# Kernel tuning notes

Hardware: AMD Instinct MI355X
Metric: run time of the kernel (lower is better)

## Reference

```python
import jax, jax.numpy as jnp
import numpy as np

N, E, IN_F, EDGE_F, HID, S = 200000, 600000, 28, 4, 128, 20000
NUM_LAYERS = 4
L = NUM_LAYERS - 1
BN_EPS = 1e-5


def setup_inputs() -> dict:
    key = jax.random.key(0)
    ks = jax.random.split(key, 20)
    p = lambda k, shape: (jax.random.normal(k, shape, dtype=jnp.float32) * 0.1)
    return {
        'x': jax.random.normal(ks[0], (N, IN_F), dtype=jnp.float32),
        'edge_index': jax.random.randint(ks[1], (2, E), 0, N),
        'edge_attr': jax.random.normal(ks[2], (E, EDGE_F), dtype=jnp.float32),
        'edge_weight': jax.random.uniform(ks[3], (E,), dtype=jnp.float32),
        'node_mask': (jax.random.uniform(ks[4], (N,)) > 0.5).astype(jnp.float32),
        'subgraphs2nodes': jax.random.randint(ks[5], (N,), 0, S),
        # layer-1 params (in_features -> hidden)
        'be1_W1': p(ks[6], (EDGE_F, IN_F)), 'be1_b1': jnp.zeros((IN_F,), jnp.float32),
        'be1_W2': p(ks[7], (IN_F, IN_F)), 'be1_b2': jnp.zeros((IN_F,), jnp.float32),
        'm1_W1': p(ks[8], (IN_F, HID)), 'm1_b1': jnp.zeros((HID,), jnp.float32),
        'm1_W2': p(ks[9], (HID, HID)), 'm1_b2': jnp.zeros((HID,), jnp.float32),
        'bn1_g': jnp.ones((HID,), jnp.float32), 'bn1_b': jnp.zeros((HID,), jnp.float32),
        'eps1': jnp.zeros((), jnp.float32),
        # layers 2..NUM_LAYERS, stacked (hidden -> hidden)
        'beW1': p(ks[10], (L, EDGE_F, HID)), 'beb1': jnp.zeros((L, HID), jnp.float32),
        'beW2': p(ks[11], (L, HID, HID)), 'beb2': jnp.zeros((L, HID), jnp.float32),
        'mW1': p(ks[12], (L, HID, HID)), 'mb1': jnp.zeros((L, HID), jnp.float32),
        'mW2': p(ks[13], (L, HID, HID)), 'mb2': jnp.zeros((L, HID), jnp.float32),
        'bng': jnp.ones((L, HID), jnp.float32), 'bnb': jnp.zeros((L, HID), jnp.float32),
        'eps': jnp.zeros((L,), jnp.float32),
    }


def _mlp2(h, W1, b1, W2, b2):
    # Linear -> ReLU -> Linear
    return jnp.dot(jax.nn.relu(jnp.dot(h, W1) + b1), W2) + b2


def _gine(x, src, dst, edge_attr, edge_weight, eps,
          beW1, beb1, beW2, beb2, W1, b1, W2, b2, g, beta):
    # bond encoder on edge features
    e = _mlp2(edge_attr, beW1, beb1, beW2, beb2)            # [E, d]
    # message: relu(x_j + e_ij) * w_ij, aggregated at dst via scatter-add
    m = jax.nn.relu(x[src] + e) * edge_weight[:, None]      # [E, d]
    aggr = jax.ops.segment_sum(m, dst, num_segments=N)      # [N, d]
    h = (1.0 + eps) * x + aggr
    # node MLP: Linear,ReLU,Linear,BN(train mode),ReLU
    h = _mlp2(h, W1, b1, W2, b2)
    mu = jnp.mean(h, axis=0)
    var = jnp.mean((h - mu) ** 2, axis=0)
    h = (h - mu) * jax.lax.rsqrt(var + BN_EPS) * g + beta
    return jax.nn.relu(h)


def reference(x, edge_index, edge_attr, edge_weight, node_mask, subgraphs2nodes,
              be1_W1, be1_b1, be1_W2, be1_b2, m1_W1, m1_b1, m1_W2, m1_b2,
              bn1_g, bn1_b, eps1,
              beW1, beb1, beW2, beb2, mW1, mb1, mW2, mb2, bng, bnb, eps):
    src, dst = edge_index[0], edge_index[1]
    h = _gine(x, src, dst, edge_attr, edge_weight, eps1,
              be1_W1, be1_b1, be1_W2, be1_b2,
              m1_W1, m1_b1, m1_W2, m1_b2, bn1_g, bn1_b)
    for i in range(L):
        h_new = _gine(h, src, dst, edge_attr, edge_weight, eps[i],
                      beW1[i], beb1[i], beW2[i], beb2[i],
                      mW1[i], mb1[i], mW2[i], mb2[i], bng[i], bnb[i])
        h = h + h_new  # residual
    # float node_mask branch + global_add_pool over subgraphs2nodes
    h = h * node_mask[:, None]
    return jax.ops.segment_sum(h, subgraphs2nodes, num_segments=S)  # [S, HID]
```

## Files before the change

### kernel.cpp

```cpp
#include <hip/hip_runtime.h>
#include <hip/hip_bf16.h>


#define BNEPS 1e-5f
#define LDA 136
#define SCAN_NB 240

typedef __attribute__((ext_vector_type(8))) short bf16x8;
typedef __attribute__((ext_vector_type(8))) unsigned short u16x8;
typedef __attribute__((ext_vector_type(4))) float f32x4;

__device__ inline short f2bf(float f) {
    __hip_bfloat16 h = __float2bfloat16(f);
    return *reinterpret_cast<short*>(&h);
}
__device__ inline unsigned short f2bfu(float f) {
    __hip_bfloat16 h = __float2bfloat16(f);
    return *reinterpret_cast<unsigned short*>(&h);
}
__device__ inline float bf2f(unsigned short u) {
    union { unsigned int i; float f; } v; v.i = ((unsigned int)u) << 16; return v.f;
}

__global__ __launch_bounds__(256) void k_prep(
    const float* __restrict__ m1W2, const float* __restrict__ beW2,
    const float* __restrict__ mW1, const float* __restrict__ mW2,
    short* __restrict__ out)
{
    __shared__ float tileS[64][65];
    int b = blockIdx.x, mat = b >> 2, t = b & 3;
    const float* Wsrc;
    if (mat == 0) Wsrc = m1W2;
    else {
        int l = (mat - 1) / 3, which = (mat - 1) % 3;
        Wsrc = (which == 0) ? beW2 + (size_t)l * 16384
             : (which == 1) ? mW1 + (size_t)l * 16384
             :                mW2 + (size_t)l * 16384;
    }
    short* dst = out + (size_t)mat * 16384;
    int tr = (t >> 1) * 64, tc = (t & 1) * 64;
    for (int i = threadIdx.x; i < 4096; i += 256) {
        int r = i >> 6, c = i & 63;
        tileS[r][c] = Wsrc[(size_t)(tr + r) * 128 + (tc + c)];
    }
    __syncthreads();
    for (int i = threadIdx.x; i < 4096; i += 256) {
        int n = i >> 6, k = i & 63;
        dst[(size_t)(tc + n) * 128 + (tr + k)] = f2bf(tileS[k][n]);
    }
}

__global__ __launch_bounds__(256) void k_prep1(
    const float* __restrict__ W1, short* __restrict__ out)
{
    for (int i = threadIdx.x; i < 128 * 32; i += 256) {
        int n = i >> 5, k = i & 31;
        out[i] = (k < 28) ? f2bf(W1[(size_t)k * 128 + n]) : (short)0;
    }
}

__global__ __launch_bounds__(256) void k_prep28(
    const float* __restrict__ W2, short* __restrict__ out)
{
    for (int i = threadIdx.x; i < 32 * 32; i += 256) {
        int n = i >> 5, k = i & 31;
        out[i] = (n < 28 && k < 28) ? f2bf(W2[(size_t)k * 28 + n]) : (short)0;
    }
}

__global__ __launch_bounds__(256) void k_prepx(
    const float* __restrict__ x, unsigned short* __restrict__ xbf, int N)
{
    int total = N * 32;
    for (int i = blockIdx.x * 256 + threadIdx.x; i < total; i += gridDim.x * 256) {
        int n = i >> 5, c = i & 31;
        xbf[i] = (c < 28) ? f2bfu(x[(size_t)n * 28 + c]) : (unsigned short)0;
    }
}

__global__ __launch_bounds__(256) void k_count(
    const int* __restrict__ ei, int* __restrict__ counts, int E)
{
    for (int e = blockIdx.x * 256 + threadIdx.x; e < E; e += gridDim.x * 256)
        atomicAdd(&counts[ei[E + e]], 1);
}

__global__ __launch_bounds__(256) void k_count2(
    const int* __restrict__ s2n, const float* __restrict__ mask,
    int* __restrict__ counts2, int N)
{
    for (int n = blockIdx.x * 256 + threadIdx.x; n < N; n += gridDim.x * 256)
        if (mask[n] != 0.f) atomicAdd(&counts2[s2n[n]], 1);
}

__global__ __launch_bounds__(256) void k_scanA(
    const int* __restrict__ counts, int* __restrict__ bsum, int N, int seg)
{
    __shared__ int red[256];
    int b = blockIdx.x;
    int lo = b * seg, hi = min(lo + seg, N);
    int s = 0;
    for (int i = lo + threadIdx.x; i < hi; i += 256) s += counts[i];
    red[threadIdx.x] = s;
    __syncthreads();
    for (int d = 128; d > 0; d >>= 1) {
        if (threadIdx.x < d) red[threadIdx.x] += red[threadIdx.x + d];
        __syncthreads();
    }
    if (threadIdx.x == 0) bsum[b] = red[0];
// ... 18 lines not shown

__global__ __launch_bounds__(256) void k_scanC(
    const int* __restrict__ counts, const int* __restrict__ bsum,
    int* __restrict__ offs, int* __restrict__ cursor, int N, int seg)
{
    __shared__ int sh[256];
    int b = blockIdx.x;
    int lo = b * seg, hi = min(lo + seg, N);
    int base = bsum[b];
    for (int t0 = lo; t0 < hi; t0 += 256) {
        int i = t0 + threadIdx.x;
        int v = (i < hi) ? counts[i] : 0;
        sh[threadIdx.x] = v;
        __syncthreads();
        for (int d = 1; d < 256; d <<= 1) {
            int t = (threadIdx.x >= d) ? sh[threadIdx.x - d] : 0;
            __syncthreads();
            sh[threadIdx.x] += t;
            __syncthreads();
        }
        int excl = base + sh[threadIdx.x] - v;
        if (i < hi) { offs[i] = excl; cursor[i] = excl; }
        int tileTotal = sh[255];
        __syncthreads();
        base += tileTotal;
    }
}

__global__ __launch_bounds__(256) void k_scatter(
    const int* __restrict__ ei, const float* __restrict__ ew,
    const float4* __restrict__ ea4,
    int* __restrict__ cursor, int2* __restrict__ pmeta,
    float4* __restrict__ pea4, int E)
{
    for (int e = blockIdx.x * 256 + threadIdx.x; e < E; e += gridDim.x * 256) {
        int d = ei[E + e];
        int pos = atomicAdd(&cursor[d], 1);
        pmeta[pos] = make_int2(ei[e], __float_as_int(ew[e]));
        pea4[pos] = ea4[e];
    }
}

__global__ __launch_bounds__(256) void k_scatter2(
    const int* __restrict__ s2n, const float* __restrict__ mask,
    int* __restrict__ cursor2, int* __restrict__ perm2, int N)
{
    for (int n = blockIdx.x * 256 + threadIdx.x; n < N; n += gridDim.x * 256)
        if (mask[n] != 0.f) {
            int pos = atomicAdd(&cursor2[s2n[n]], 1);
            perm2[pos] = n;
        }
}

__global__ __launch_bounds__(256) void k_emsg(
    const float4* __restrict__ pea4,
    const float* __restrict__ W1, const float* __restrict__ b1,
    const short* __restrict__ W2t, const float* __restrict__ b2,
    unsigned short* __restrict__ emsg, const int* __restrict__ offs,
    int n0, int n1)
{
    __shared__ short Bs[128 * LDA];
    __shared__ short As[64 * LDA];
    __shared__ float eas[64][4];
    int e0 = offs[n0], e1 = offs[n1];
    int tid = threadIdx.x;
    for (int i = tid; i < 2048; i += 256) {
        int n = (i * 8) >> 7, k = (i * 8) & 127;
        *(bf16x8*)&Bs[n * LDA + k] = *(const bf16x8*)&W2t[i * 8];
    }
    int j = tid & 127, half = tid >> 7;
    float w10 = W1[j], w11 = W1[128 + j], w12 = W1[256 + j], w13 = W1[384 + j];
    float b1j = b1[j];
    int w = tid >> 6, lane = tid & 63;
    int l15 = lane & 15, quad = lane >> 4;
    __syncthreads();

    int numTiles = (e1 - e0 + 63) >> 6;
    for (int tile = blockIdx.x; tile < numTiles; tile += gridDim.x) {
        int base = e0 + tile * 64;
        __syncthreads();
        if (tid < 64) {
            int k = base + tid;
            float4 a = make_float4(0.f, 0.f, 0.f, 0.f);
            if (k < e1) a = pea4[k];
            eas[tid][0] = a.x; eas[tid][1] = a.y; eas[tid][2] = a.z; eas[tid][3] = a.w;
        }
        __syncthreads();
        #pragma unroll
        for (int q = 0; q < 32; ++q) {
            int e = half * 32 + q;
            float t = fmaf(eas[e][0], w10, fmaf(eas[e][1], w11,
                      fmaf(eas[e][2], w12, fmaf(eas[e][3], w13, b1j))));
            As[e * LDA + j] = f2bf(fmaxf(t, 0.f));
        }
        __syncthreads();
        f32x4 acc[8];
        #pragma unroll
        for (int nt = 0; nt < 8; ++nt) acc[nt] = (f32x4){0.f, 0.f, 0.f, 0.f};
        #pragma unroll
        for (int kt = 0; kt < 4; ++kt) {
            bf16x8 af = *(bf16x8*)&As[(w * 16 + l15) * LDA + kt * 32 + quad * 8];
            #pragma unroll
            for (int nt = 0; nt < 8; ++nt) {
                bf16x8 bf = *(bf16x8*)&Bs[(nt * 16 + l15) * LDA + kt * 32 + quad * 8];
                acc[nt] = __builtin_amdgcn_mfma_f32_16x16x32_bf16(af, bf, acc[nt], 0, 0, 0);
            }
        }
        #pragma unroll
        for (int nt = 0; nt < 8; ++nt) {
            int col = nt * 16 + l15;
            float b2c = b2[col];
            #pragma unroll
            for (int r = 0; r < 4; ++r) {
                int row = w * 16 + quad * 4 + r;
                As[row * LDA + col] = f2bf(acc[nt][r] + b2c);
            }
        }
        __syncthreads();
        #pragma unroll
        for (int kk = 0; kk < 4; ++kk) {
            int i = tid + kk * 256;
            int row = (i * 8) >> 7, col = (i * 8) & 127;
            int gr = base + row;
            if (gr < e1)
                *(bf16x8*)&emsg[(size_t)(gr - e0) * 128 + col] = *(bf16x8*)&As[row * LDA + col];
        }
    }
}

__global__ __launch_bounds__(256) void k_emsg28_mm(
    const float4* __restrict__ pea4,
    const float* __restrict__ W1, const float* __restrict__ b1,
    const short* __restrict__ W2t28,
    const float* __restrict__ b2,
    unsigned short* __restrict__ emsg28, int E)
{
    __shared__ short Bs[32 * 40];
    __shared__ short As[64 * 40];
    __shared__ float eas[64][4];
    __shared__ float b2s[32];
    int tid = threadIdx.x;
    for (int i = tid; i < 32 * 32; i += 256) {
        int n = i >> 5, k = i & 31;
        Bs[n * 40 + k] = W2t28[i];
    }
    if (tid < 32) b2s[tid] = (tid < 28) ? b2[tid] : 0.f;
    int j = tid & 31, sub = tid >> 5;
    float w10 = 0.f, w11 = 0.f, w12 = 0.f, w13 = 0.f, b1j = 0.f;
    if (j < 28) { w10 = W1[j]; w11 = W1[28 + j]; w12 = W1[56 + j]; w13 = W1[84 + j]; b1j = b1[j]; }
    int w = tid >> 6, lane = tid & 63;
    int l15 = lane & 15, quad = lane >> 4;
    __syncthreads();

    int numTiles = (E + 63) >> 6;
    for (int tile = blockIdx.x; tile < numTiles; tile += gridDim.x) {
        int base = tile * 64;
        __syncthreads();
        if (tid < 64) {
            int k = base + tid;
            float4 a = (k < E) ? pea4[k] : make_float4(0.f, 0.f, 0.f, 0.f);
            eas[tid][0] = a.x; eas[tid][1] = a.y; eas[tid][2] = a.z; eas[tid][3] = a.w;
        }
        __syncthreads();
        #pragma unroll
        for (int q = 0; q < 8; ++q) {
            int e = q * 8 + sub;
            float t = fmaf(eas[e][0], w10, fmaf(eas[e][1], w11,
                      fmaf(eas[e][2], w12, fmaf(eas[e][3], w13, b1j))));
            As[e * 40 + j] = (j < 28) ? f2bf(fmaxf(t, 0.f)) : (short)0;
        }
        __syncthreads();
        f32x4 acc[2];
        acc[0] = (f32x4){0.f, 0.f, 0.f, 0.f};
        acc[1] = (f32x4){0.f, 0.f, 0.f, 0.f};
        bf16x8 af = *(bf16x8*)&As[(w * 16 + l15) * 40 + quad * 8];
        #pragma unroll
        for (int nt = 0; nt < 2; ++nt) {
            bf16x8 bf = *(bf16x8*)&Bs[(nt * 16 + l15) * 40 + quad * 8];
// ... 20 lines not shown
__global__ __launch_bounds__(256) void k_gather(
    const unsigned short* __restrict__ h, const int* __restrict__ offs,
    const int2* __restrict__ pmeta, const unsigned short* __restrict__ emsg,
    unsigned short* __restrict__ a0,
    const float* __restrict__ epsp, int epsIdx,
    int n0, int n1)
{
    int grp = threadIdx.x >> 5, lane = threadIdx.x & 31;
    int n = n0 + blockIdx.x * 8 + grp;
    if (n >= n1) return;
    int e0 = offs[n0];
    int k0 = offs[n], k1 = offs[n + 1];
    float s = 1.0f + epsp[epsIdx];
    ushort4 hv0 = *(const ushort4*)&h[(size_t)n * 128 + lane * 4];
    float m0 = s * bf2f(hv0.x), m1 = s * bf2f(hv0.y);
    float m2 = s * bf2f(hv0.z), m3 = s * bf2f(hv0.w);
    for (int k = k0; k < k1; ++k) {
        int2 mt = pmeta[k];
        float w = __int_as_float(mt.y);
        ushort4 ev = *(const ushort4*)&emsg[(size_t)(k - e0) * 128 + lane * 4];
        ushort4 hv = *(const ushort4*)&h[(size_t)mt.x * 128 + lane * 4];
        m0 += fmaxf(bf2f(hv.x) + bf2f(ev.x), 0.f) * w;
        m1 += fmaxf(bf2f(hv.y) + bf2f(ev.y), 0.f) * w;
        m2 += fmaxf(bf2f(hv.z) + bf2f(ev.z), 0.f) * w;
        m3 += fmaxf(bf2f(hv.w) + bf2f(ev.w), 0.f) * w;
    }
    ushort4 o;
    o.x = f2bfu(m0); o.y = f2bfu(m1); o.z = f2bfu(m2); o.w = f2bfu(m3);
    *(ushort4*)&a0[(size_t)n * 128 + lane * 4] = o;
}

__global__ __launch_bounds__(256) void k_gather28(
    const float* __restrict__ x, const unsigned short* __restrict__ xbf,
    const int* __restrict__ offs,
    const int2* __restrict__ pmeta, const unsigned short* __restrict__ emsg28,
    const float* __restrict__ eps1, float* __restrict__ u28, int N)
{
    int grp = threadIdx.x >> 5, lane = threadIdx.x & 31;
    int n = blockIdx.x * 8 + grp;
    if (n >= N || lane >= 28) return;
    float s = 1.0f + eps1[0];
    int k0 = offs[n], k1 = offs[n + 1];
    float m = 0.f;
    for (int k = k0; k < k1; ++k) {
        int2 mt = pmeta[k];
        float w = __int_as_float(mt.y);
        float e = bf2f(emsg28[(size_t)k * 28 + lane]);
        float xs = bf2f(xbf[(size_t)mt.x * 32 + lane]);
        m += fmaxf(xs + e, 0.f) * w;
    }
    u28[(size_t)n * 28 + lane] = fmaf(s, x[(size_t)n * 28 + lane], m);
}

__global__ __launch_bounds__(512) void k_mlp(
    const unsigned short* __restrict__ src, const short* __restrict__ Wt1,
    const float* __restrict__ b1, const short* __restrict__ Wt2,
    const float* __restrict__ b2, unsigned short* __restrict__ dst,
    float* __restrict__ stats, int N)
{
    __shared__ short Bs1[128 * LDA];
    __shared__ short Bs2[128 * LDA];
    __shared__ short As[128 * LDA];
    __shared__ float sstat[256];
    int tid = threadIdx.x;
    for (int i = tid; i < 2048; i += 512) {
        int n = (i * 8) >> 7, k = (i * 8) & 127;
        *(bf16x8*)&Bs1[n * LDA + k] = *(const bf16x8*)&Wt1[i * 8];
        *(bf16x8*)&Bs2[n * LDA + k] = *(const bf16x8*)&Wt2[i * 8];
    }
    if (tid < 256) sstat[tid] = 0.f;
    int w = tid >> 6, lane = tid & 63;
    int l15 = lane & 15, quad = lane >> 4;
    int cg = w >> 2;
    int rb = (w & 3) * 32;
    __syncthreads();

    bf16x8 B1f[4][4], B2f[4][4];
    float b1r[4], b2r[4];
    #pragma unroll
    for (int nt = 0; nt < 4; ++nt) {
        int col = cg * 64 + nt * 16 + l15;
        b1r[nt] = b1[col]; b2r[nt] = b2[col];
        #pragma unroll
        for (int kt = 0; kt < 4; ++kt) {
            B1f[nt][kt] = *(bf16x8*)&Bs1[col * LDA + kt * 32 + quad * 8];
            B2f[nt][kt] = *(bf16x8*)&Bs2[col * LDA + kt * 32 + quad * 8];
        }
    }
    float lsum[2][4], lsq[2][4];
    #pragma unroll
    for (int rg = 0; rg < 2; ++rg)
        #pragma unroll
        for (int nt = 0; nt < 4; ++nt) { lsum[rg][nt] = 0.f; lsq[rg][nt] = 0.f; }

    int numTiles = (N + 127) >> 7;
    for (int tile = blockIdx.x; tile < numTiles; tile += gridDim.x) {
        int base = tile * 128;
        __syncthreads();
        #pragma unroll
        for (int kk = 0; kk < 4; ++kk) {
            int i = tid + kk * 512;
            int row = (i * 8) >> 7, col = (i * 8) & 127;
            int rr = base + row;
            bf16x8 v;
            if (rr < N) v = *(const bf16x8*)&src[(size_t)rr * 128 + col];
            else        v = (bf16x8){0,0,0,0,0,0,0,0};
            *(bf16x8*)&As[row * LDA + col] = v;
        }
        __syncthreads();
        f32x4 acc[2][4];
        #pragma unroll
        for (int rg = 0; rg < 2; ++rg)
            #pragma unroll
            for (int nt = 0; nt < 4; ++nt) acc[rg][nt] = (f32x4){0.f, 0.f, 0.f, 0.f};
        #pragma unroll
        for (int rg = 0; rg < 2; ++rg) {
            #pragma unroll
            for (int kt = 0; kt < 4; ++kt) {
                bf16x8 af = *(bf16x8*)&As[(rb + rg * 16 + l15) * LDA + kt * 32 + quad * 8];
                #pragma unroll
                for (int nt = 0; nt < 4; ++nt)
                    acc[rg][nt] = __builtin_amdgcn_mfma_f32_16x16x32_bf16(af, B1f[nt][kt], acc[rg][nt], 0, 0, 0);
            }
        }
        __syncthreads();
        #pragma unroll
        for (int rg = 0; rg < 2; ++rg)
            #pragma unroll
            for (int nt = 0; nt < 4; ++nt) {
                int col = cg * 64 + nt * 16 + l15;
                #pragma unroll
                for (int r = 0; r < 4; ++r)
                    As[(rb + rg * 16 + quad * 4 + r) * LDA + col] =
                        f2bf(fmaxf(acc[rg][nt][r] + b1r[nt], 0.f));
            }
        __syncthreads();
        #pragma unroll
        for (int rg = 0; rg < 2; ++rg)
            #pragma unroll
            for (int nt = 0; nt < 4; ++nt) acc[rg][nt] = (f32x4){0.f, 0.f, 0.f, 0.f};
        #pragma unroll
        for (int rg = 0; rg < 2; ++rg) {
            #pragma unroll
            for (int kt = 0; kt < 4; ++kt) {
                bf16x8 af = *(bf16x8*)&As[(rb + rg * 16 + l15) * LDA + kt * 32 + quad * 8];
                #pragma unroll
                for (int nt = 0; nt < 4; ++nt)
                    acc[rg][nt] = __builtin_amdgcn_mfma_f32_16x16x32_bf16(af, B2f[nt][kt], acc[rg][nt], 0, 0, 0);
            }
        }
        __syncthreads();
        #pragma unroll
        for (int rg = 0; rg < 2; ++rg)
            #pragma unroll
            for (int nt = 0; nt < 4; ++nt) {
                int col = cg * 64 + nt * 16 + l15;
                int row0 = base + rb + rg * 16 + quad * 4;
                #pragma unroll
                for (int r = 0; r < 4; ++r) {
                    float z = acc[rg][nt][r] + b2r[nt];
                    if (row0 + r < N) { lsum[rg][nt] += z; lsq[rg][nt] = fmaf(z, z, lsq[rg][nt]); }
                    As[(rb + rg * 16 + quad * 4 + r) * LDA + col] = f2bf(z);
                }
            }
        __syncthreads();
        #pragma unroll
        for (int kk = 0; kk < 4; ++kk) {
            int i = tid + kk * 512;
            int row = (i * 8) >> 7, col = (i * 8) & 127;
            int rr = base + row;
            if (rr < N)
                *(bf16x8*)&dst[(size_t)rr * 128 + col] = *(bf16x8*)&As[row * LDA + col];
        }
    }
    #pragma unroll
    for (int nt = 0; nt < 4; ++nt) {
        int col = cg * 64 + nt * 16 + l15;
        atomicAdd(&sstat[col], lsum[0][nt] + lsum[1][nt]);
        atomicAdd(&sstat[128 + col], lsq[0][nt] + lsq[1][nt]);
    }
    __syncthreads();
    if (tid < 256) atomicAdd(&stats[tid], sstat[tid]);
}

__global__ __launch_bounds__(512) void k_mlp1(
    const float* __restrict__ u28, const short* __restrict__ Wt1p,
    const float* __restrict__ b1, const short* __restrict__ Wt2,
    const float* __restrict__ b2, unsigned short* __restrict__ dst,
    float* __restrict__ stats, int N)
{
    __shared__ short Bs1[128 * 40];
    __shared__ short Bs2[128 * LDA];
    __shared__ short As[128 * LDA];
    __shared__ short A28[128 * 40];
    __shared__ float sstat[256];
    int tid = threadIdx.x;
    for (int i = tid; i < 128 * 32; i += 512) {
        int n = i >> 5, k = i & 31;
        Bs1[n * 40 + k] = Wt1p[i];
    }
    for (int i = tid; i < 2048; i += 512) {
        int n = (i * 8) >> 7, k = (i * 8) & 127;
        *(bf16x8*)&Bs2[n * LDA + k] = *(const bf16x8*)&Wt2[i * 8];
    }
    {
        int r = tid >> 2, c = tid & 3;
        if (r < 128) A28[r * 40 + 28 + c] = 0;
    }
    if (tid < 256) sstat[tid] = 0.f;
    int w = tid >> 6, lane = tid & 63;
    int l15 = lane & 15, quad = lane >> 4;
    int cg = w >> 2, rb = (w & 3) * 32;
    __syncthreads();

    bf16x8 B1f[4], B2f[4][4];
    float b1r[4], b2r[4];
    #pragma unroll
    for (int nt = 0; nt < 4; ++nt) {
        int col = cg * 64 + nt * 16 + l15;
        b1r[nt] = b1[col]; b2r[nt] = b2[col];
        B1f[nt] = *(bf16x8*)&Bs1[col * 40 + quad * 8];
        #pragma unroll
        for (int kt = 0; kt < 4; ++kt)
            B2f[nt][kt] = *(bf16x8*)&Bs2[col * LDA + kt * 32 + quad * 8];
    }
    float lsum[2][4], lsq[2][4];
    #pragma unroll
    for (int rg = 0; rg < 2; ++rg)
        #pragma unroll
        for (int nt = 0; nt < 4; ++nt) { lsum[rg][nt] = 0.f; lsq[rg][nt] = 0.f; }

    int numTiles = (N + 127) >> 7;
    for (int tile = blockIdx.x; tile < numTiles; tile += gridDim.x) {
        int base = tile * 128;
        __syncthreads();
        for (int i = tid; i < 128 * 28; i += 512) {
            int row = i / 28, col = i - row * 28;
            int rr = base + row;
            A28[row * 40 + col] = (rr < N) ? f2bf(u28[(size_t)rr * 28 + col]) : (short)0;
        }
        __syncthreads();
        f32x4 acc[2][4];
        #pragma unroll
        for (int rg = 0; rg < 2; ++rg)
            #pragma unroll
            for (int nt = 0; nt < 4; ++nt) acc[rg][nt] = (f32x4){0.f, 0.f, 0.f, 0.f};
        #pragma unroll
        for (int rg = 0; rg < 2; ++rg) {
            bf16x8 af = *(bf16x8*)&A28[(rb + rg * 16 + l15) * 40 + quad * 8];
            #pragma unroll
            for (int nt = 0; nt < 4; ++nt)
                acc[rg][nt] = __builtin_amdgcn_mfma_f32_16x16x32_bf16(af, B1f[nt], acc[rg][nt], 0, 0, 0);
        }
        #pragma unroll
        for (int rg = 0; rg < 2; ++rg)
            #pragma unroll
            for (int nt = 0; nt < 4; ++nt) {
                int col = cg * 64 + nt * 16 + l15;
                #pragma unroll
                for (int r = 0; r < 4; ++r)
                    As[(rb + rg * 16 + quad * 4 + r) * LDA + col] =
                        f2bf(fmaxf(acc[rg][nt][r] + b1r[nt], 0.f));
            }
        __syncthreads();
        #pragma unroll
        for (int rg = 0; rg < 2; ++rg)
            #pragma unroll
            for (int nt = 0; nt < 4; ++nt) acc[rg][nt] = (f32x4){0.f, 0.f, 0.f, 0.f};
        #pragma unroll
        for (int rg = 0; rg < 2; ++rg) {
            #pragma unroll
            for (int kt = 0; kt < 4; ++kt) {
                bf16x8 af = *(bf16x8*)&As[(rb + rg * 16 + l15) * LDA + kt * 32 + quad * 8];
                #pragma unroll
                for (int nt = 0; nt < 4; ++nt)
                    acc[rg][nt] = __builtin_amdgcn_mfma_f32_16x16x32_bf16(af, B2f[nt][kt], acc[rg][nt], 0, 0, 0);
            }
        }
        __syncthreads();
        #pragma unroll
        for (int rg = 0; rg < 2; ++rg)
            #pragma unroll
            for (int nt = 0; nt < 4; ++nt) {
                int col = cg * 64 + nt * 16 + l15;
                int row0 = base + rb + rg * 16 + quad * 4;
                #pragma unroll
                for (int r = 0; r < 4; ++r) {
                    float z = acc[rg][nt][r] + b2r[nt];
                    if (row0 + r < N) { lsum[rg][nt] += z; lsq[rg][nt] = fmaf(z, z, lsq[rg][nt]); }
                    As[(rb + rg * 16 + quad * 4 + r) * LDA + col] = f2bf(z);
                }
            }
        __syncthreads();
        #pragma unroll
        for (int kk = 0; kk < 4; ++kk) {
            int i = tid + kk * 512;
            int row = (i * 8) >> 7, col = (i * 8) & 127;
            int rr = base + row;
            if (rr < N)
                *(bf16x8*)&dst[(size_t)rr * 128 + col] = *(bf16x8*)&As[row * LDA + col];
        }
    }
    #pragma unroll
    for (int nt = 0; nt < 4; ++nt) {
        int col = cg * 64 + nt * 16 + l15;
        atomicAdd(&sstat[col], lsum[0][nt] + lsum[1][nt]);
        atomicAdd(&sstat[128 + col], lsq[0][nt] + lsq[1][nt]);
    }
    __syncthreads();
    if (tid < 256) atomicAdd(&stats[tid], sstat[tid]);
}

__global__ __launch_bounds__(128) void k_stats(
    const float* __restrict__ stats, const float* __restrict__ g,
    const float* __restrict__ b, float* __restrict__ ss, float invN)
{
    int j = threadIdx.x;
    float mu  = stats[j] * invN;
    float var = fmaf(stats[128 + j], invN, -mu * mu);
    float sc  = rsqrtf(fmaxf(var, 0.f) + BNEPS) * g[j];
    ss[j] = sc;
    ss[128 + j] = fmaf(-mu, sc, b[j]);
}

__global__ __launch_bounds__(256) void k_bn(
    const unsigned short* __restrict__ z, const float* __restrict__ ss,
    unsigned short* __restrict__ h, int residual, int N)
{
    int idx8 = blockIdx.x * 256 + threadIdx.x;
    int stride = gridDim.x * 256;
    int c0 = (idx8 & 15) * 8;
    float scl[8], sht[8];
    #pragma unroll
    for (int r = 0; r < 8; ++r) { scl[r] = ss[c0 + r]; sht[r] = ss[128 + c0 + r]; }
    int total8 = N * 16;
    for (; idx8 < total8; idx8 += stride) {
        int n = idx8 >> 4;
        u16x8 z8 = *(const u16x8*)&z[(size_t)n * 128 + c0];
        float hn[8];
        #pragma unroll
        for (int r = 0; r < 8; ++r)
            hn[r] = fmaxf(fmaf(bf2f(z8[r]), scl[r], sht[r]), 0.f);
        if (residual) {
            u16x8 h8 = *(const u16x8*)&h[(size_t)n * 128 + c0];
            #pragma unroll
            for (int r = 0; r < 8; ++r) hn[r] += bf2f(h8[r]);
        }
        u16x8 o;
        #pragma unroll
        for (int r = 0; r < 8; ++r) o[r] = f2bfu(hn[r]);
        *(u16x8*)&h[(size_t)n * 128 + c0] = o;
    }
}

__global__ __launch_bounds__(256) void k_poolbn(
    const unsigned short* __restrict__ z, const unsigned short* __restrict__ hprev,
    const float* __restrict__ ss, const int* __restrict__ offs2,
    const int* __restrict__ perm2, float* __restrict__ out, int S)
{
    int w = threadIdx.x >> 6, lane = threadIdx.x & 63;
// ... 77 lines not shown
    if (ws_size < need) return;

    unsigned short* h    = (unsigned short*)(ws + offH);
    unsigned short* a0   = (unsigned short*)(ws + offA0);
    unsigned short* emsg = (unsigned short*)(ws + offEm);
    float* u28    = (float*)(ws + offA0);
    unsigned short* xbf = (unsigned short*)(ws + offA0 + 26214400);
    float* stats  = (float*)(ws + offStats);
    float* ssbuf  = (float*)(ws + offSS);
    short* wts    = (short*)(ws + offWts);
    short* w1p    = wts + 10 * 16384;
    short* w2p28  = w1p + 4096;
    int*   counts = (int*)(ws + offCounts);
    int*   offs   = (int*)(ws + offOffs);
    int*   cursor = (int*)(ws + offCursor);
    int2*  pmeta  = (int2*)(ws + offPmeta);
    float4* pea4  = (float4*)(ws + offPea);
    int*   bsum   = (int*)(ws + offBsum);
    int*   cnt2   = (int*)(ws + offCnt2);
    int*   offs2  = (int*)(ws + offOffs2);
    int*   cur2   = (int*)(ws + offCur2);
    int*   perm2  = (int*)(ws + offPerm2);
    const float4* ea4 = (const float4*)ea;

    hipMemsetAsync(stats, 0, 4 * 256 * sizeof(float), stream);
    hipMemsetAsync(counts, 0, (size_t)N * sizeof(int), stream);
    hipMemsetAsync(cnt2, 0, (size_t)S * sizeof(int), stream);

    k_prep<<<40, 256, 0, stream>>>(m1W2, beW2, mW1, mW2, wts);
    k_prep1<<<1, 256, 0, stream>>>(m1W1, w1p);
    k_prep28<<<1, 256, 0, stream>>>(be1W2, w2p28);
    k_prepx<<<512, 256, 0, stream>>>(x, xbf, N);

    const int seg = (N + SCAN_NB - 1) / SCAN_NB;
    k_count<<<1024, 256, 0, stream>>>(ei, counts, E);
    k_scanA<<<SCAN_NB, 256, 0, stream>>>(counts, bsum, N, seg);
    k_scanB<<<1, 256, 0, stream>>>(bsum, SCAN_NB, offs, N);
    k_scanC<<<SCAN_NB, 256, 0, stream>>>(counts, bsum, offs, cursor, N, seg);
    k_scatter<<<1024, 256, 0, stream>>>(ei, ew, ea4, cursor, pmeta, pea4, E);

    const int seg2 = (S + SCAN_NB - 1) / SCAN_NB;
    k_count2<<<512, 256, 0, stream>>>(s2n, mask, cnt2, N);
    k_scanA<<<SCAN_NB, 256, 0, stream>>>(cnt2, bsum, S, seg2);
    k_scanB<<<1, 256, 0, stream>>>(bsum, SCAN_NB, offs2, S);
    k_scanC<<<SCAN_NB, 256, 0, stream>>>(cnt2, bsum, offs2, cur2, S, seg2);
    k_scatter2<<<512, 256, 0, stream>>>(s2n, mask, cur2, perm2, N);

    auto wt_be = [&](int l) { return wts + (size_t)(1 + 3 * l + 0) * 16384; };
    auto wt_m1 = [&](int l) { return wts + (size_t)(1 + 3 * l + 1) * 16384; };
    auto wt_m2 = [&](int l) { return wts + (size_t)(1 + 3 * l + 2) * 16384; };

    k_emsg28_mm<<<2048, 256, 0, stream>>>(pea4, be1W1, be1b1, w2p28, be1b2, emsg, E);
    k_gather28<<<(N + 7) / 8, 256, 0, stream>>>(x, xbf, offs, pmeta, emsg, eps1, u28, N);
    k_mlp1<<<512, 512, 0, stream>>>(u28, w1p, m1b1, wts , m1b2, h, stats, N);
    k_stats<<<1, 128, 0, stream>>>(stats, bn1g, bn1b, ssbuf, invN);
    k_bn<<<2048, 256, 0, stream>>>(h, ssbuf, h, 0, N);

    for (int l = 0; l < 3; ++l) {
        for (int c = 0; c < 2; ++c) {
            int n0 = (c == 0) ? 0 : NS;
            int n1 = (c == 0) ? NS : N;
            k_emsg<<<2048, 256, 0, stream>>>(pea4,
                beW1 + (size_t)l * 512, beb1 + (size_t)l * 128,
                wt_be(l), beb2 + (size_t)l * 128, emsg, offs, n0, n1);
            k_gather<<<(n1 - n0 + 7) / 8, 256, 0, stream>>>(h, offs, pmeta, emsg, a0,
                epsL, l, n0, n1);
        }
        k_mlp<<<512, 512, 0, stream>>>(a0, wt_m1(l), mb1 + (size_t)l * 128,
                                       wt_m2(l), mb2 + (size_t)l * 128, a0,
                                       stats + 256 * (l + 1), N);
        k_stats<<<1, 128, 0, stream>>>(stats + 256 * (l + 1),
            bng + (size_t)l * 128, bnb + (size_t)l * 128, ssbuf, invN);
        if (l < 2) {
            k_bn<<<2048, 256, 0, stream>>>(a0, ssbuf, h, 1, N);
        }
    }

    k_poolbn<<<(S + 3) / 4, 256, 0, stream>>>(a0, h, ssbuf, offs2, perm2,
                                              (float*)d_out, S);
}
```

Before: 1.041 ms.

## Pre-swizzle weights into MFMA fragment order and restructure MLP/edge-encoder kernels

Weights are rewritten at prep time into the exact per-lane MFMA B-fragment order, so kernels copy them linearly into LDS and read conflict-free contiguous fragments instead of keeping them in registers or using padded rows. The node MLP kernels now have each wave own 32 full rows across all 128 columns, double-buffer the next tile's input in registers, and drop most block barriers because waves only touch their own rows. The edge encoder computes the first layer per wave via shuffles with no shared staging or barriers. Grid sizes are halved for 256-row tiles and occupancy hints are added, at the cost of more registers and larger LDS footprint.

Result: no change. 1.030 ms (-1.1%).

```diff
diff --git a/kernel.cpp b/kernel.cpp
--- a/kernel.cpp
+++ b/kernel.cpp
@@ -21,6 +21,7 @@
 __device__ inline float bf2f(unsigned short u) {
     union { unsigned int i; float f; } v; v.i = ((unsigned int)u) << 16; return v.f;
 }
+
 
 __global__ __launch_bounds__(256) void k_prep(
     const float* __restrict__ m1W2, const float* __restrict__ beW2,
@@ -45,16 +46,20 @@
     }
     __syncthreads();
     for (int i = threadIdx.x; i < 4096; i += 256) {
-        int n = i >> 6, k = i & 63;
-        dst[(size_t)(tc + n) * 128 + (tr + k)] = f2bf(tileS[k][n]);
+        int kl = i & 63, nl = i >> 6;
+        int n = tc + nl, k = tr + kl;
+        int fo = (((n >> 4) * 4 + (k >> 5)) * 64 + (((k >> 3) & 3) * 16 + (n & 15))) * 8 + (k & 7);
+        dst[fo] = f2bf(tileS[kl][nl]);
     }
 }
 
 __global__ __launch_bounds__(256) void k_prep1(
     const float* __restrict__ W1, short* __restrict__ out)
 {
-    for (int i = threadIdx.x; i < 128 * 32; i += 256) {
-        int n = i >> 5, k = i & 31;
+    for (int i = threadIdx.x; i < 4096; i += 256) {
+        int j = i & 7, sub = (i >> 3) & 63, nt = i >> 9;
+        int quad = sub >> 4, l15 = sub & 15;
+        int n = nt * 16 + l15, k = quad * 8 + j;
         out[i] = (k < 28) ? f2bf(W1[(size_t)k * 128 + n]) : (short)0;
     }
 }
@@ -179,78 +184,73 @@
         }
 }
 
-__global__ __launch_bounds__(256) void k_emsg(
+__global__ __launch_bounds__(256, 3) void k_emsg(
     const float4* __restrict__ pea4,
     const float* __restrict__ W1, const float* __restrict__ b1,
-    const short* __restrict__ W2t, const float* __restrict__ b2,
+    const short* __restrict__ W2f, const float* __restrict__ b2,
     unsigned short* __restrict__ emsg, const int* __restrict__ offs,
     int n0, int n1)
 {
-    __shared__ short Bs[128 * LDA];
     __shared__ short As[64 * LDA];
-    __shared__ float eas[64][4];
+    __shared__ short Bs[16384];
     int e0 = offs[n0], e1 = offs[n1];
     int tid = threadIdx.x;
-    for (int i = tid; i < 2048; i += 256) {
-        int n = (i * 8) >> 7, k = (i * 8) & 127;
-        *(bf16x8*)&Bs[n * LDA + k] = *(const bf16x8*)&W2t[i * 8];
-    }
-    int j = tid & 127, half = tid >> 7;
-    float w10 = W1[j], w11 = W1[128 + j], w12 = W1[256 + j], w13 = W1[384 + j];
-    float b1j = b1[j];
     int w = tid >> 6, lane = tid & 63;
     int l15 = lane & 15, quad = lane >> 4;
+    int rb = w * 16;
+    for (int i = tid; i < 2048; i += 256)
+        *(bf16x8*)&Bs[i * 8] = *(const bf16x8*)&W2f[i * 8];
+    int c2 = lane * 2;
+    float w1a[4], w1b[4];
+    #pragma unroll
+    for (int a = 0; a < 4; ++a) { w1a[a] = W1[a * 128 + c2]; w1b[a] = W1[a * 128 + c2 + 1]; }
+    float b1a = b1[c2], b1b = b1[c2 + 1];
+    float b2r[8];
+    #pragma unroll
+    for (int nt = 0; nt < 8; ++nt) b2r[nt] = b2[nt * 16 + l15];
     __syncthreads();
 
+    const float* peaf = (const float*)pea4;
     int numTiles = (e1 - e0 + 63) >> 6;
     for (int tile = blockIdx.x; tile < numTiles; tile += gridDim.x) {
         int base = e0 + tile * 64;
-        __syncthreads();
-        if (tid < 64) {
-            int k = base + tid;
-            float4 a = make_float4(0.f, 0.f, 0.f, 0.f);
-            if (k < e1) a = pea4[k];
-            eas[tid][0] = a.x; eas[tid][1] = a.y; eas[tid][2] = a.z; eas[tid][3] = a.w;
-        }
-        __syncthreads();
-        #pragma unroll
-        for (int q = 0; q < 32; ++q) {
-            int e = half * 32 + q;
-            float t = fmaf(eas[e][0], w10, fmaf(eas[e][1], w11,
-                      fmaf(eas[e][2], w12, fmaf(eas[e][3], w13, b1j))));
-            As[e * LDA + j] = f2bf(fmaxf(t, 0.f));
-        }
-        __syncthreads();
+        int eidx = base + rb + (lane >> 2);
+        float v = (eidx < e1) ? peaf[(size_t)(base + rb) * 4 + lane] : 0.f;
+        #pragma unroll
+        for (int e = 0; e < 16; ++e) {
+            float a0v = __shfl(v, e * 4 + 0);
+            float a1v = __shfl(v, e * 4 + 1);
+            float a2v = __shfl(v, e * 4 + 2);
+            float a3v = __shfl(v, e * 4 + 3);
+            float t0 = fmaf(a0v, w1a[0], fmaf(a1v, w1a[1], fmaf(a2v, w1a[2], fmaf(a3v, w1a[3], b1a))));
+            float t1 = fmaf(a0v, w1b[0], fmaf(a1v, w1b[1], fmaf(a2v, w1b[2], fmaf(a3v, w1b[3], b1b))));
+            unsigned int pk = ((unsigned int)f2bfu(fmaxf(t1, 0.f)) << 16) | f2bfu(fmaxf(t0, 0.f));
+        *(unsigned int*)&As[(rb + e) * LDA + c2] = pk;
+        }
         f32x4 acc[8];
         #pragma unroll
         for (int nt = 0; nt < 8; ++nt) acc[nt] = (f32x4){0.f, 0.f, 0.f, 0.f};
         #pragma unroll
         for (int kt = 0; kt < 4; ++kt) {
-            bf16x8 af = *(bf16x8*)&As[(w * 16 + l15) * LDA + kt * 32 + quad * 8];
+            bf16x8 af = *(bf16x8*)&As[(rb + l15) * LDA + kt * 32 + quad * 8];
             #pragma unroll
             for (int nt = 0; nt < 8; ++nt) {
-                bf16x8 bf = *(bf16x8*)&Bs[(nt * 16 + l15) * LDA + kt * 32 + quad * 8];
+                bf16x8 bf = *(const bf16x8*)&Bs[((nt * 4 + kt) * 64 + lane) * 8];
                 acc[nt] = __builtin_amdgcn_mfma_f32_16x16x32_bf16(af, bf, acc[nt], 0, 0, 0);
             }
         }
         #pragma unroll
         for (int nt = 0; nt < 8; ++nt) {
-            int col = nt * 16 + l15;
-            float b2c = b2[col];
-            #pragma unroll
-            for (int r = 0; r < 4; ++r) {
-                int row = w * 16 + quad * 4 + r;
-                As[row * LDA + col] = f2bf(acc[nt][r] + b2c);
-            }
-        }
-        __syncthreads();
-        #pragma unroll
-        for (int kk = 0; kk < 4; ++kk) {
-            int i = tid + kk * 256;
-            int row = (i * 8) >> 7, col = (i * 8) & 127;
-            int gr = base + row;
+            #pragma unroll
+            for (int r = 0; r < 4; ++r)
+                As[(rb + quad * 4 + r) * LDA + nt * 16 + l15] = f2bf(acc[nt][r] + b2r[nt]);
+        }
+        #pragma unroll
+        for (int it = 0; it < 4; ++it) {
+            int arow = rb + it * 4 + quad;
+            int gr = base + arow;
             if (gr < e1)
-                *(bf16x8*)&emsg[(size_t)(gr - e0) * 128 + col] = *(bf16x8*)&As[row * LDA + col];
+                *(bf16x8*)&emsg[(size_t)(gr - e0) * 128 + l15 * 8] = *(bf16x8*)&As[arow * LDA + l15 * 8];
         }
     }
 }
@@ -377,260 +377,268 @@
     u28[(size_t)n * 28 + lane] = fmaf(s, x[(size_t)n * 28 + lane], m);
 }
 
-__global__ __launch_bounds__(512) void k_mlp(
-    const unsigned short* __restrict__ src, const short* __restrict__ Wt1,
-    const float* __restrict__ b1, const short* __restrict__ Wt2,
+__global__ __launch_bounds__(512, 2) void k_mlp(
+    const unsigned short* __restrict__ src, const short* __restrict__ W1f,
+    const float* __restrict__ b1, const short* __restrict__ W2f,
     const float* __restrict__ b2, unsigned short* __restrict__ dst,
     float* __restrict__ stats, int N)
 {
-    __shared__ short Bs1[128 * LDA];
-    __shared__ short Bs2[128 * LDA];
-    __shared__ short As[128 * LDA];
+    __shared__ short As[256 * LDA];
+    __shared__ short Bs1[16384];
+    __shared__ short Bs2[16384];
     __shared__ float sstat[256];
     int tid = threadIdx.x;
     for (int i = tid; i < 2048; i += 512) {
-        int n = (i * 8) >> 7, k = (i * 8) & 127;
-        *(bf16x8*)&Bs1[n * LDA + k] = *(const bf16x8*)&Wt1[i * 8];
-        *(bf16x8*)&Bs2[n * LDA + k] = *(const bf16x8*)&Wt2[i * 8];
+        *(bf16x8*)&Bs1[i * 8] = *(const bf16x8*)&W1f[i * 8];
+        *(bf16x8*)&Bs2[i * 8] = *(const bf16x8*)&W2f[i * 8];
     }
     if (tid < 256) sstat[tid] = 0.f;
     int w = tid >> 6, lane = tid & 63;
     int l15 = lane & 15, quad = lane >> 4;
-    int cg = w >> 2;
-    int rb = (w & 3) * 32;
+    int rb = w * 32;
+    float b1r[8], b2r[8], lsum[8], lsq[8];
+    #pragma unroll
+    for (int nt = 0; nt < 8; ++nt) {
+        b1r[nt] = b1[nt * 16 + l15]; b2r[nt] = b2[nt * 16 + l15];
+        lsum[nt] = 0.f; lsq[nt] = 0.f;
+    }
+    int numTiles = (N + 255) >> 8;
+    bf16x8 st[8];
+    {
+        int tile = blockIdx.x;
+        if (tile < numTiles) {
+            int base = tile * 256;
+            #pragma unroll
+            for (int kk = 0; kk < 8; ++kk) {
+                int i = tid + kk * 512;
+                int rr = base + (i >> 4);
+                st[kk] = (rr < N) ? *(const bf16x8*)&src[(size_t)rr * 128 + (i & 15) * 8]
+                                  : (bf16x8){0, 0, 0, 0, 0, 0, 0, 0};
+            }
+        }
+    }
     __syncthreads();
 
-    bf16x8 B1f[4][4], B2f[4][4];
-    float b1r[4], b2r[4];
-    #pragma unroll
-    for (int nt = 0; nt < 4; ++nt) {
-        int col = cg * 64 + nt * 16 + l15;
-        b1r[nt] = b1[col]; b2r[nt] = b2[col];
+    for (int tile = blockIdx.x; tile < numTiles; tile += gridDim.x) {
+        int base = tile * 256;
+        #pragma unroll
+        for (int kk = 0; kk < 8; ++kk) {
+            int i = tid + kk * 512;
+            *(bf16x8*)&As[(i >> 4) * LDA + (i & 15) * 8] = st[kk];
+        }
+        int tnext = tile + gridDim.x;
+        if (tnext < numTiles) {
+            int bn = tnext * 256;
+            #pragma unroll
+            for (int kk = 0; kk < 8; ++kk) {
+                int i = tid + kk * 512;
+                int rr = bn + (i >> 4);
+                st[kk] = (rr < N) ? *(const bf16x8*)&src[(size_t)rr * 128 + (i & 15) * 8]
+                                  : (bf16x8){0, 0, 0, 0, 0, 0, 0, 0};
+            }
+        }
+        __syncthreads();
+        f32x4 acc[2][8];
+        #pragma unroll
+        for (int rg = 0; rg < 2; ++rg)
+            #pragma unroll
+            for (int nt = 0; nt < 8; ++nt) acc[rg][nt] = (f32x4){0.f, 0.f, 0.f, 0.f};
         #pragma unroll
         for (int kt = 0; kt < 4; ++kt) {
-            B1f[nt][kt] = *(bf16x8*)&Bs1[col * LDA + kt * 32 + quad * 8];
-            B2f[nt][kt] = *(bf16x8*)&Bs2[col * LDA + kt * 32 + quad * 8];
-        }
-    }
-    float lsum[2][4], lsq[2][4];
-    #pragma unroll
-    for (int rg = 0; rg < 2; ++rg)
-        #pragma unroll
-        for (int nt = 0; nt < 4; ++nt) { lsum[rg][nt] = 0.f; lsq[rg][nt] = 0.f; }
-
-    int numTiles = (N + 127) >> 7;
-    for (int tile = blockIdx.x; tile < numTiles; tile += gridDim.x) {
-        int base = tile * 128;
-        __syncthreads();
-        #pragma unroll
-        for (int kk = 0; kk < 4; ++kk) {
-            int i = tid + kk * 512;
-            int row = (i * 8) >> 7, col = (i * 8) & 127;
-            int rr = base + row;
-            bf16x8 v;
-            if (rr < N) v = *(const bf16x8*)&src[(size_t)rr * 128 + col];
-            else        v = (bf16x8){0,0,0,0,0,0,0,0};
-            *(bf16x8*)&As[row * LDA + col] = v;
-        }
-        __syncthreads();
-        f32x4 acc[2][4];
+            bf16x8 af0 = *(bf16x8*)&As[(rb + l15) * LDA + kt * 32 + quad * 8];
+            bf16x8 af1 = *(bf16x8*)&As[(rb + 16 + l15) * LDA + kt * 32 + quad * 8];
+            #pragma unroll
+            for (int nt = 0; nt < 8; ++nt) {
+                bf16x8 bf = *(const bf16x8*)&Bs1[((nt * 4 + kt) * 64 + lane) * 8];
+                acc[0][nt] = __builtin_amdgcn_mfma_f32_16x16x32_bf16(af0, bf, acc[0][nt], 0, 0, 0);
+                acc[1][nt] = __builtin_amdgcn_mfma_f32_16x16x32_bf16(af1, bf, acc[1][nt], 0, 0, 0);
+            }
+        }
         #pragma unroll
         for (int rg = 0; rg < 2; ++rg)
             #pragma unroll
-            for (int nt = 0; nt < 4; ++nt) acc[rg][nt] = (f32x4){0.f, 0.f, 0.f, 0.f};
-        #pragma unroll
-        for (int rg = 0; rg < 2; ++rg) {
-            #pragma unroll
-            for (int kt = 0; kt < 4; ++kt) {
-                bf16x8 af = *(bf16x8*)&As[(rb + rg * 16 + l15) * LDA + kt * 32 + quad * 8];
-                #pragma unroll
-                for (int nt = 0; nt < 4; ++nt)
-                    acc[rg][nt] = __builtin_amdgcn_mfma_f32_16x16x32_bf16(af, B1f[nt][kt], acc[rg][nt], 0, 0, 0);
-            }
-        }
-        __syncthreads();
-        #pragma unroll
-        for (int rg = 0; rg < 2; ++rg)
-            #pragma unroll
-            for (int nt = 0; nt < 4; ++nt) {
-                int col = cg * 64 + nt * 16 + l15;
+            for (int nt = 0; nt < 8; ++nt)
                 #pragma unroll
                 for (int r = 0; r < 4; ++r)
-                    As[(rb + rg * 16 + quad * 4 + r) * LDA + col] =
+                    As[(rb + rg * 16 + quad * 4 + r) * LDA + nt * 16 + l15] =
                         f2bf(fmaxf(acc[rg][nt][r] + b1r[nt], 0.f));
-            }
-        __syncthreads();
         #pragma unroll
         for (int rg = 0; rg < 2; ++rg)
             #pragma unroll
-            for (int nt = 0; nt < 4; ++nt) acc[rg][nt] = (f32x4){0.f, 0.f, 0.f, 0.f};
-        #pragma unroll
-        for (int rg = 0; rg < 2; ++rg) {
-            #pragma unroll
-            for (int kt = 0; kt < 4; ++kt) {
-                bf16x8 af = *(bf16x8*)&As[(rb + rg * 16 + l15) * LDA + kt * 32 + quad * 8];
-                #pragma unroll
-                for (int nt = 0; nt < 4; ++nt)
-                    acc[rg][nt] = __builtin_amdgcn_mfma_f32_16x16x32_bf16(af, B2f[nt][kt], acc[rg][nt], 0, 0, 0);
-            }
-        }
-        __syncthreads();
+            for (int nt = 0; nt < 8; ++nt) acc[rg][nt] = (f32x4){0.f, 0.f, 0.f, 0.f};
+        #pragma unroll
+        for (int kt = 0; kt < 4; ++kt) {
+            bf16x8 af0 = *(bf16x8*)&As[(rb + l15) * LDA + kt * 32 + quad * 8];
+            bf16x8 af1 = *(bf16x8*)&As[(rb + 16 + l15) * LDA + kt * 32 + quad * 8];
+            #pragma unroll
+            for (int nt = 0; nt < 8; ++nt) {
+                bf16x8 bf = *(const bf16x8*)&Bs2[((nt * 4 + kt) * 64 + lane) * 8];
+                acc[0][nt] = __builtin_amdgcn_mfma_f32_16x16x32_bf16(af0, bf, acc[0][nt], 0, 0, 0);
+                acc[1][nt] = __builtin_amdgcn_mfma_f32_16x16x32_bf16(af1, bf, acc[1][nt], 0, 0, 0);
+            }
+        }
         #pragma unroll
         for (int rg = 0; rg < 2; ++rg)
             #pragma unroll
-            for (int nt = 0; nt < 4; ++nt) {
-                int col = cg * 64 + nt * 16 + l15;
+            for (int nt = 0; nt < 8; ++nt) {
                 int row0 = base + rb + rg * 16 + quad * 4;
                 #pragma unroll
                 for (int r = 0; r < 4; ++r) {
                     float z = acc[rg][nt][r] + b2r[nt];
-                    if (row0 + r < N) { lsum[rg][nt] += z; lsq[rg][nt] = fmaf(z, z, lsq[rg][nt]); }
-                    As[(rb + rg * 16 + quad * 4 + r) * LDA + col] = f2bf(z);
+                    if (row0 + r < N) { lsum[nt] += z; lsq[nt] = fmaf(z, z, lsq[nt]); }
+                    As[(rb + rg * 16 + quad * 4 + r) * LDA + nt * 16 + l15] = f2bf(z);
                 }
             }
-        __syncthreads();
-        #pragma unroll
-        for (int kk = 0; kk < 4; ++kk) {
-            int i = tid + kk * 512;
-            int row = (i * 8) >> 7, col = (i * 8) & 127;
-            int rr = base + row;
+        #pragma unroll
+        for (int it = 0; it < 8; ++it) {
+            int arow = rb + it * 4 + quad;
+            int rr = base + arow;
             if (rr < N)
-                *(bf16x8*)&dst[(size_t)rr * 128 + col] = *(bf16x8*)&As[row * LDA + col];
-        }
+                *(bf16x8*)&dst[(size_t)rr * 128 + l15 * 8] = *(bf16x8*)&As[arow * LDA + l15 * 8];
+        }
+        __syncthreads();
     }
     #pragma unroll
-    for (int nt = 0; nt < 4; ++nt) {
-        int col = cg * 64 + nt * 16 + l15;
-        atomicAdd(&sstat[col], lsum[0][nt] + lsum[1][nt]);
-        atomicAdd(&sstat[128 + col], lsq[0][nt] + lsq[1][nt]);
+    for (int nt = 0; nt < 8; ++nt) {
+        atomicAdd(&sstat[nt * 16 + l15], lsum[nt]);
+        atomicAdd(&sstat[128 + nt * 16 + l15], lsq[nt]);
     }
     __syncthreads();
     if (tid < 256) atomicAdd(&stats[tid], sstat[tid]);
 }
 
-__global__ __launch_bounds__(512) void k_mlp1(
-    const float* __restrict__ u28, const short* __restrict__ Wt1p,
-    const float* __restrict__ b1, const short* __restrict__ Wt2,
+__global__ __launch_bounds__(512, 2) void k_mlp1(
+    const float* __restrict__ u28, const short* __restrict__ W1f,
+    const float* __restrict__ b1, const short* __restrict__ W2f,
     const float* __restrict__ b2, unsigned short* __restrict__ dst,
     float* __restrict__ stats, int N)
 {
-    __shared__ short Bs1[128 * 40];
-    __shared__ short Bs2[128 * LDA];
-    __shared__ short As[128 * LDA];
-    __shared__ short A28[128 * 40];
+    __shared__ short A28[256 * 40];
+    __shared__ short As[256 * LDA];
+    __shared__ short Bs1[4096];
+    __shared__ short Bs2[16384];
     __shared__ float sstat[256];
     int tid = threadIdx.x;
-    for (int i = tid; i < 128 * 32; i += 512) {
-        int n = i >> 5, k = i & 31;
-        Bs1[n * 40 + k] = Wt1p[i];
-    }
-    for (int i = tid; i < 2048; i += 512) {
-        int n = (i * 8) >> 7, k = (i * 8) & 127;
-        *(bf16x8*)&Bs2[n * LDA + k] = *(const bf16x8*)&Wt2[i * 8];
-    }
-    {
-        int r = tid >> 2, c = tid & 3;
-        if (r < 128) A28[r * 40 + 28 + c] = 0;
+    if (tid < 512) {
+        int i = tid;
+        *(bf16x8*)&Bs1[i * 8] = *(const bf16x8*)&W1f[i * 8];
+    }
+    for (int i = tid; i < 2048; i += 512)
+        *(bf16x8*)&Bs2[i * 8] = *(const bf16x8*)&W2f[i * 8];
+    for (int i = tid; i < 1024; i += 512) {
+        int row = i >> 2, c = 28 + (i & 3);
+        A28[row * 40 + c] = 0;
     }
     if (tid < 256) sstat[tid] = 0.f;
     int w = tid >> 6, lane = tid & 63;
     int l15 = lane & 15, quad = lane >> 4;
-    int cg = w >> 2, rb = (w & 3) * 32;
+    int rb = w * 32;
+    float b1r[8], b2r[8], lsum[8], lsq[8];
+    #pragma unroll
+    for (int nt = 0; nt < 8; ++nt) {
+        b1r[nt] = b1[nt * 16 + l15]; b2r[nt] = b2[nt * 16 + l15];
+        lsum[nt] = 0.f; lsq[nt] = 0.f;
+    }
+    int numTiles = (N + 255) >> 8;
+    float stf[14];
+    {
+        int tile = blockIdx.x;
+        if (tile < numTiles) {
+            int base = tile * 256;
+            #pragma unroll
+            for (int kk = 0; kk < 14; ++kk) {
+                int idx = tid + kk * 512;
+                int row = idx / 28, col = idx - row * 28;
+                int rr = base + row;
+                stf[kk] = (rr < N) ? u28[(size_t)rr * 28 + col] : 0.f;
+            }
+        }
+    }
     __syncthreads();
 
-    bf16x8 B1f[4], B2f[4][4];
-    float b1r[4], b2r[4];
-    #pragma unroll
-    for (int nt = 0; nt < 4; ++nt) {
-        int col = cg * 64 + nt * 16 + l15;
-        b1r[nt] = b1[col]; b2r[nt] = b2[col];
-        B1f[nt] = *(bf16x8*)&Bs1[col * 40 + quad * 8];
-        #pragma unroll
-        for (int kt = 0; kt < 4; ++kt)
-            B2f[nt][kt] = *(bf16x8*)&Bs2[col * LDA + kt * 32 + quad * 8];
-    }
-    float lsum[2][4], lsq[2][4];
-    #pragma unroll
-    for (int rg = 0; rg < 2; ++rg)
-        #pragma unroll
-        for (int nt = 0; nt < 4; ++nt) { lsum[rg][nt] = 0.f; lsq[rg][nt] = 0.f; }
-
-    int numTiles = (N + 127) >> 7;
     for (int tile = blockIdx.x; tile < numTiles; tile += gridDim.x) {
-        int base = tile * 128;
-        __syncthreads();
-        for (int i = tid; i < 128 * 28; i += 512) {
-            int row = i / 28, col = i - row * 28;
-            int rr = base + row;
-            A28[row * 40 + col] = (rr < N) ? f2bf(u28[(size_t)rr * 28 + col]) : (short)0;
-        }
-        __syncthreads();
-        f32x4 acc[2][4];
+        int base = tile * 256;
+        #pragma unroll
+        for (int kk = 0; kk < 14; ++kk) {
+            int idx = tid + kk * 512;
+            int row = idx / 28, col = idx - row * 28;
+            A28[row * 40 + col] = f2bf(stf[kk]);
+        }
+        int tnext = tile + gridDim.x;
+        if (tnext < numTiles) {
+            int bn = tnext * 256;
+            #pragma unroll
+            for (int kk = 0; kk < 14; ++kk) {
+                int idx = tid + kk * 512;
+                int row = idx / 28, col = idx - row * 28;
+                int rr = bn + row;
+                stf[kk] = (rr < N) ? u28[(size_t)rr * 28 + col] : 0.f;
+            }
+        }
+        __syncthreads();
+        f32x4 acc[2][8];
         #pragma unroll
         for (int rg = 0; rg < 2; ++rg)
             #pragma unroll
-            for (int nt = 0; nt < 4; ++nt) acc[rg][nt] = (f32x4){0.f, 0.f, 0.f, 0.f};
-        #pragma unroll
-        for (int rg = 0; rg < 2; ++rg) {
-            bf16x8 af = *(bf16x8*)&A28[(rb + rg * 16 + l15) * 40 + quad * 8];
-            #pragma unroll
-            for (int nt = 0; nt < 4; ++nt)
-                acc[rg][nt] = __builtin_amdgcn_mfma_f32_16x16x32_bf16(af, B1f[nt], acc[rg][nt], 0, 0, 0);
+            for (int nt = 0; nt < 8; ++nt) acc[rg][nt] = (f32x4){0.f, 0.f, 0.f, 0.f};
+        {
+            bf16x8 af0 = *(bf16x8*)&A28[(rb + l15) * 40 + quad * 8];
+            bf16x8 af1 = *(bf16x8*)&A28[(rb + 16 + l15) * 40 + quad * 8];
+            #pragma unroll
+            for (int nt = 0; nt < 8; ++nt) {
+                bf16x8 bf = *(const bf16x8*)&Bs1[(nt * 64 + lane) * 8];
+                acc[0][nt] = __builtin_amdgcn_mfma_f32_16x16x32_bf16(af0, bf, acc[0][nt], 0, 0, 0);
+                acc[1][nt] = __builtin_amdgcn_mfma_f32_16x16x32_bf16(af1, bf, acc[1][nt], 0, 0, 0);
+            }
         }
         #pragma unroll
         for (int rg = 0; rg < 2; ++rg)
             #pragma unroll
-            for (int nt = 0; nt < 4; ++nt) {
-                int col = cg * 64 + nt * 16 + l15;
+            for (int nt = 0; nt < 8; ++nt)
                 #pragma unroll
                 for (int r = 0; r < 4; ++r)
-                    As[(rb + rg * 16 + quad * 4 + r) * LDA + col] =
+                    As[(rb + rg * 16 + quad * 4 + r) * LDA + nt * 16 + l15] =
                         f2bf(fmaxf(acc[rg][nt][r] + b1r[nt], 0.f));
-            }
-        __syncthreads();
         #pragma unroll
         for (int rg = 0; rg < 2; ++rg)
             #pragma unroll
-            for (int nt = 0; nt < 4; ++nt) acc[rg][nt] = (f32x4){0.f, 0.f, 0.f, 0.f};
-        #pragma unroll
-        for (int rg = 0; rg < 2; ++rg) {
-            #pragma unroll
-            for (int kt = 0; kt < 4; ++kt) {
-                bf16x8 af = *(bf16x8*)&As[(rb + rg * 16 + l15) * LDA + kt * 32 + quad * 8];
-                #pragma unroll
-                for (int nt = 0; nt < 4; ++nt)
-                    acc[rg][nt] = __builtin_amdgcn_mfma_f32_16x16x32_bf16(af, B2f[nt][kt], acc[rg][nt], 0, 0, 0);
-            }
-        }
-        __syncthreads();
+            for (int nt = 0; nt < 8; ++nt) acc[rg][nt] = (f32x4){0.f, 0.f, 0.f, 0.f};
+        #pragma unroll
+        for (int kt = 0; kt < 4; ++kt) {
+            bf16x8 af0 = *(bf16x8*)&As[(rb + l15) * LDA + kt * 32 + quad * 8];
+            bf16x8 af1 = *(bf16x8*)&As[(rb + 16 + l15) * LDA + kt * 32 + quad * 8];
+            #pragma unroll
+            for (int nt = 0; nt < 8; ++nt) {
+                bf16x8 bf = *(const bf16x8*)&Bs2[((nt * 4 + kt) * 64 + lane) * 8];
+                acc[0][nt] = __builtin_amdgcn_mfma_f32_16x16x32_bf16(af0, bf, acc[0][nt], 0, 0, 0);
+                acc[1][nt] = __builtin_amdgcn_mfma_f32_16x16x32_bf16(af1, bf, acc[1][nt], 0, 0, 0);
+            }
+        }
         #pragma unroll
         for (int rg = 0; rg < 2; ++rg)
             #pragma unroll
-            for (int nt = 0; nt < 4; ++nt) {
-                int col = cg * 64 + nt * 16 + l15;
+            for (int nt = 0; nt < 8; ++nt) {
                 int row0 = base + rb + rg * 16 + quad * 4;
                 #pragma unroll
                 for (int r = 0; r < 4; ++r) {
                     float z = acc[rg][nt][r] + b2r[nt];
-                    if (row0 + r < N) { lsum[rg][nt] += z; lsq[rg][nt] = fmaf(z, z, lsq[rg][nt]); }
-                    As[(rb + rg * 16 + quad * 4 + r) * LDA + col] = f2bf(z);
+                    if (row0 + r < N) { lsum[nt] += z; lsq[nt] = fmaf(z, z, lsq[nt]); }
+                    As[(rb + rg * 16 + quad * 4 + r) * LDA + nt * 16 + l15] = f2bf(z);
                 }
             }
-        __syncthreads();
-        #pragma unroll
-        for (int kk = 0; kk < 4; ++kk) {
-            int i = tid + kk * 512;
-            int row = (i * 8) >> 7, col = (i * 8) & 127;
-            int rr = base + row;
+        #pragma unroll
+        for (int it = 0; it < 8; ++it) {
+            int arow = rb + it * 4 + quad;
+            int rr = base + arow;
             if (rr < N)
-                *(bf16x8*)&dst[(size_t)rr * 128 + col] = *(bf16x8*)&As[row * LDA + col];
-        }
+                *(bf16x8*)&dst[(size_t)rr * 128 + l15 * 8] = *(bf16x8*)&As[arow * LDA + l15 * 8];
+        }
+        __syncthreads();
     }
     #pragma unroll
-    for (int nt = 0; nt < 4; ++nt) {
-        int col = cg * 64 + nt * 16 + l15;
-        atomicAdd(&sstat[col], lsum[0][nt] + lsum[1][nt]);
-        atomicAdd(&sstat[128 + col], lsq[0][nt] + lsq[1][nt]);
+    for (int nt = 0; nt < 8; ++nt) {
+        atomicAdd(&sstat[nt * 16 + l15], lsum[nt]);
+        atomicAdd(&sstat[128 + nt * 16 + l15], lsq[nt]);
     }
     __syncthreads();
     if (tid < 256) atomicAdd(&stats[tid], sstat[tid]);
@@ -814,7 +822,7 @@
 
     k_emsg28_mm<<<2048, 256, 0, stream>>>(pea4, be1W1, be1b1, w2p28, be1b2, emsg, E);
     k_gather28<<<(N + 7) / 8, 256, 0, stream>>>(x, xbf, offs, pmeta, emsg, eps1, u28, N);
-    k_mlp1<<<512, 512, 0, stream>>>(u28, w1p, m1b1, wts , m1b2, h, stats, N);
+    k_mlp1<<<256, 512, 0, stream>>>(u28, w1p, m1b1, wts , m1b2, h, stats, N);
     k_stats<<<1, 128, 0, stream>>>(stats, bn1g, bn1b, ssbuf, invN);
     k_bn<<<2048, 256, 0, stream>>>(h, ssbuf, h, 0, N);
 
@@ -828,7 +836,7 @@
             k_gather<<<(n1 - n0 + 7) / 8, 256, 0, stream>>>(h, offs, pmeta, emsg, a0,
                 epsL, l, n0, n1);
         }
-        k_mlp<<<512, 512, 0, stream>>>(a0, wt_m1(l), mb1 + (size_t)l * 128,
+        k_mlp<<<256, 512, 0, stream>>>(a0, wt_m1(l), mb1 + (size_t)l * 128,
                                        wt_m2(l), mb2 + (size_t)l * 128, a0,
                                        stats + 256 * (l + 1), N);
         k_stats<<<1, 128, 0, stream>>>(stats + 256 * (l + 1),
```
